# Performance work log

Hardware: AMD Instinct MI355X
Metric: run time of the kernel (lower is better)

## Reference

```python
import jax, jax.numpy as jnp
import numpy as np

B, P = 4, 50000
D_IN, COND = 3, 48
# layer l: in IN_DIMS[l] -> out OUT_DIMS[l]; dims=[3,256*8,257], skip at layer index 4
IN_DIMS  = [D_IN + COND, 256, 256, 256, 256, 256, 256, 256, 256]
OUT_DIMS = [256, 256, 256, 253, 256, 256, 256, 256, 257]
N_LIN = 9
INV_SQRT2 = np.float32(1.0 / np.sqrt(2.0))


def softplus_beta100(x):
    return jax.nn.softplus(100.0 * x) * 0.01


def setup_inputs() -> dict:
    key = jax.random.key(0)
    ks = jax.random.split(key, 2 + 2 * N_LIN)
    inp = {
        "input": jax.random.normal(ks[0], (B, P, D_IN), dtype=jnp.float32),
        "cond_pose": jax.random.normal(ks[1], (B, COND), dtype=jnp.float32),
    }
    for l in range(N_LIN):
        scale = np.float32(np.sqrt(2.0 / OUT_DIMS[l]))  # geometry-style init scale
        inp[f"W{l}"] = jax.random.normal(ks[2 + 2 * l], (OUT_DIMS[l], IN_DIMS[l]), dtype=jnp.float32) * scale
        inp[f"b{l}"] = jnp.zeros((OUT_DIMS[l],), dtype=jnp.float32)
    return inp


def reference(input, cond_pose,
              W0, b0, W1, b1, W2, b2, W3, b3, W4, b4, W5, b5, W6, b6, W7, b7, W8, b8):
    Ws = [W0, W1, W2, W3, W4, W5, W6, W7, W8]
    bs = [b0, b1, b2, b3, b4, b5, b6, b7, b8]
    nb, npnt, nd = input.shape
    x_in = input.reshape(nb * npnt, nd)                                   # (N, 3)
    c = jnp.broadcast_to(cond_pose[:, None, :], (nb, npnt, COND)).reshape(nb * npnt, COND)
    x = jnp.concatenate([x_in, c], axis=-1)                               # cond concat at layer 0
    for l in range(N_LIN):
        if l == 4:  # skip connection: concat raw input, scaled by 1/sqrt(2)
            x = jnp.concatenate([x, x_in], axis=-1) * INV_SQRT2
        x = x @ Ws[l].T + bs[l]
        if l < N_LIN - 1:
            x = softplus_beta100(x)
    return x.reshape(nb, npnt, -1)                                        # (B, P, 257)
```

## Files before the change

kernel.cpp:

```cpp
#include <hip/hip_runtime.h>


typedef __attribute__((ext_vector_type(8))) short bf16x8;
typedef __attribute__((ext_vector_type(4))) float f32x4;
typedef __attribute__((ext_vector_type(2))) float f32x2;

#define PPTS 50000

__device__ __forceinline__ short f2bf(float f) {
    union { float f; unsigned u; } v; v.f = f;
    unsigned r = v.u + 0x7fffu + ((v.u >> 16) & 1u);
    return (short)(r >> 16);
}

__device__ __forceinline__ unsigned cvt_pk_bf16(float lo, float hi) {
    unsigned r;
    asm("v_cvt_pk_bf16_f32 %0, %1, %2" : "=v"(r) : "v"(lo), "v"(hi));
    return r;
}

__device__ __forceinline__ void bar_lgkm() {
    asm volatile("s_waitcnt lgkmcnt(0)" ::: "memory");
    __builtin_amdgcn_s_barrier();
    __builtin_amdgcn_sched_barrier(0);
}

__device__ __forceinline__ f32x2 sp100_pair(f32x2 y) {
    const f32x2 A2 = {6.9314718e-3f, 6.9314718e-3f};
    const f32x2 B2 = {-3.11522e-3f, -3.11522e-3f};
    const f32x2 C2 = {9.8829e-4f,  9.8829e-4f};
    const f32x2 K2 = {-144.26950408889634f, -144.26950408889634f};
    const f32x2 Z2 = {0.0f, 0.0f};
    f32x2 m = __builtin_elementwise_abs(y) * K2;
    f32x2 e = {__builtin_amdgcn_exp2f(m.x), __builtin_amdgcn_exp2f(m.y)};
    f32x2 t = __builtin_elementwise_fma(C2, e, B2);
    t = __builtin_elementwise_fma(t, e, A2);
    return __builtin_elementwise_fma(e, t, __builtin_elementwise_max(y, Z2));
}

__device__ __forceinline__ int xswz(int row) {
    return (((row & 7) ^ (5 * ((row >> 3) & 1))) << 4);
}
__device__ __forceinline__ short* xaddr(short* base, int row, int col) {
    int off = ((row << 9) + (col << 1)) ^ xswz(row);
    return (short*)((char*)base + off);
}
__device__ __forceinline__ const short* xaddrc(const short* base, int row, int col) {
    int off = ((row << 9) + (col << 1)) ^ xswz(row);
    return (const short*)((const char*)base + off);
}

__global__ void prep_kernel(
    const float* __restrict__ W0, const float* __restrict__ W1, const float* __restrict__ W2,
    const float* __restrict__ W3, const float* __restrict__ W4, const float* __restrict__ W5,
    const float* __restrict__ W6, const float* __restrict__ W7, const float* __restrict__ W8,
    short* __restrict__ wbf)
{
    const int gid = blockIdx.x * blockDim.x + threadIdx.x;
    if (gid >= 68096) return;
    int l, cid; const float* Wsrc;
    if      (gid <  2048) { l = 0; cid = gid;         Wsrc = W0; }
    else if (gid < 10240) { l = 1; cid = gid -  2048; Wsrc = W1; }
    else if (gid < 18432) { l = 2; cid = gid - 10240; Wsrc = W2; }
    else if (gid < 26624) { l = 3; cid = gid - 18432; Wsrc = W3; }
    else if (gid < 34816) { l = 4; cid = gid - 26624; Wsrc = W4; }
    else if (gid < 43008) { l = 5; cid = gid - 34816; Wsrc = W5; }
    else if (gid < 51200) { l = 6; cid = gid - 43008; Wsrc = W6; }
    else if (gid < 59392) { l = 7; cid = gid - 51200; Wsrc = W7; }
    else                  { l = 8; cid = gid - 59392; Wsrc = W8; }
    const int NR   = (l == 3) ? 253 : ((l == 8) ? 257 : 256);
    const int KR   = (l == 0) ? 51 : 256;
    const int klog = (l == 0) ? 1 : 3;
    const float sc = (l == 4) ? 0.70710678f : 1.0f;
    const int lane  = cid & 63;
    const int tile  = cid >> 6;
    const int ntile = tile >> klog;
    const int ktile = tile & ((1 << klog) - 1);
    const int n  = ntile * 16 + (lane & 15);
    const int k0 = ktile * 32 + ((lane >> 4) << 3);
    bf16x8 v;
#pragma unroll
    for (int j = 0; j < 8; ++j) {
        int k = k0 + j;
        float f = (n < NR && k < KR) ? Wsrc[n * KR + k] * sc : 0.0f;
        v[j] = f2bf(f);
    }
    ((bf16x8*)wbf)[gid] = v;
}

template<int KSTEPS, int MODE>
__device__ __forceinline__ void layer_fwd(short* xb,
    const bf16x8* __restrict__ wl, const bf16x8* __restrict__ wlnext,
    const float* __restrict__ bias, int lane, int wid, bf16x8 (&apre)[4])
{
    const int prow = lane & 15;
    const int kg   = (lane >> 4) << 3;
    const int rb4  = (lane >> 4) << 2;
    f32x4 acc[4][4];
#pragma unroll
    for (int nii = 0; nii < 4; ++nii) {
        const int cb = (wid * 4 + nii) * 16 + rb4;
        f32x4 bv;
        if (MODE == 1 && cb == 252) { f32x4 tb = {bias[252], 0.f, 0.f, 0.f}; bv = tb; }
        else bv = *(const f32x4*)(bias + cb);
#pragma unroll
        for (int mi = 0; mi < 4; ++mi)
            acc[mi][nii] = bv;
    }
#pragma unroll 2
    for (int ks = 0; ks < KSTEPS; ++ks) {
        bf16x8 a[4], b[4];
#pragma unroll
        for (int nii = 0; nii < 4; ++nii)
            a[nii] = (ks == 0) ? apre[nii]
                               : wl[((wid * 4 + nii) * KSTEPS + ks) * 64 + lane];
#pragma unroll
        for (int mi = 0; mi < 4; ++mi)
            b[mi] = *(const bf16x8*)xaddrc(xb, mi * 16 + prow, ks * 32 + kg);
#pragma unroll
        for (int mi = 0; mi < 4; ++mi)
#pragma unroll
            for (int nii = 0; nii < 4; ++nii)
                acc[mi][nii] = __builtin_amdgcn_mfma_f32_16x16x32_bf16(
                    a[nii], b[mi], acc[mi][nii], 0, 0, 0);
    }
#pragma unroll
    for (int nii = 0; nii < 4; ++nii)
        apre[nii] = wlnext[(wid * 4 + nii) * 512 + lane];
#pragma unroll
    for (int nii = 0; nii < 4; ++nii)
#pragma unroll
        for (int mi = 0; mi < 4; ++mi) {
            f32x2 y0 = {acc[mi][nii][0], acc[mi][nii][1]};
            f32x2 y1 = {acc[mi][nii][2], acc[mi][nii][3]};
            f32x2 r0 = sp100_pair(y0);
            f32x2 r1 = sp100_pair(y1);
            acc[mi][nii][0] = r0.x; acc[mi][nii][1] = r0.y;
            acc[mi][nii][2] = r1.x; acc[mi][nii][3] = r1.y;
        }
    bar_lgkm();
#pragma unroll
    for (int nii = 0; nii < 4; ++nii) {
        const int cb = (wid * 4 + nii) * 16 + rb4;
#pragma unroll
        for (int mi = 0; mi < 4; ++mi) {
            unsigned p01 = cvt_pk_bf16(acc[mi][nii][0], acc[mi][nii][1]);
            unsigned p23 = cvt_pk_bf16(acc[mi][nii][2], acc[mi][nii][3]);
            if (MODE == 1 && cb == 252) {
                *xaddr(xb, mi * 16 + prow, 252) = (short)(p01 & 0xffff);
            } else {
                uint2 pk; pk.x = p01; pk.y = p23;
                *(uint2*)xaddr(xb, mi * 16 + prow, cb) = pk;
            }
        }
    }
}

__global__ __launch_bounds__(256, 3) void net_kernel(
    const float* __restrict__ xin, const float* __restrict__ cond,
    const bf16x8* __restrict__ W,
    const float* __restrict__ b0, const float* __restrict__ b1, const float* __restrict__ b2,
    const float* __restrict__ b3, const float* __restrict__ b4, const float* __restrict__ b5,
    const float* __restrict__ b6, const float* __restrict__ b7, const float* __restrict__ b8,
    float* __restrict__ out)
{
    __shared__ short xb[64 * 256];
    const int t    = threadIdx.x;
    const int pt0  = blockIdx.x * 64;
    const int lane = t & 63;
    const int wid  = t >> 6;

    bf16x8 apre[4];
#pragma unroll
    for (int nii = 0; nii < 4; ++nii)
        apre[nii] = W[(wid * 4 + nii) * 128 + lane];

    float sk[3] = {0.f, 0.f, 0.f};
    if (t < 64) {
#pragma unroll
        for (int c = 0; c < 3; ++c)
            sk[c] = xin[(pt0 + t) * 3 + c];
    }

    {
        const int row   = t >> 2;
        const int c0    = (t & 3) << 4;
        const int point = pt0 + row;
        const int batch = point / PPTS;
        const float* xp = xin + point * 3;
        const float* cp = cond + batch * 48;
#pragma unroll
        for (int h = 0; h < 2; ++h) {
            bf16x8 v;
#pragma unroll
            for (int i = 0; i < 8; ++i) {
                int c = c0 + h * 8 + i;
                float f = (c < 3) ? xp[c] : ((c < 51) ? cp[c - 3] : 0.0f);
                v[i] = f2bf(f);
            }
            *(bf16x8*)xaddr(xb, row, c0 + h * 8) = v;
        }
    }
    bar_lgkm();

    layer_fwd<2, 0>(xb, W +     0, W +  2048, b0, lane, wid, apre); bar_lgkm();
    layer_fwd<8, 0>(xb, W +  2048, W + 10240, b1, lane, wid, apre); bar_lgkm();
    layer_fwd<8, 0>(xb, W + 10240, W + 18432, b2, lane, wid, apre); bar_lgkm();
    layer_fwd<8, 1>(xb, W + 18432, W + 26624, b3, lane, wid, apre);
    if (t < 64) {
#pragma unroll
        for (int c = 0; c < 3; ++c)
            *xaddr(xb, t, 253 + c) = f2bf(sk[c]);
    }
    bar_lgkm();
    layer_fwd<8, 0>(xb, W + 26624, W + 34816, b4, lane, wid, apre); bar_lgkm();
    layer_fwd<8, 0>(xb, W + 34816, W + 43008, b5, lane, wid, apre); bar_lgkm();
    layer_fwd<8, 0>(xb, W + 43008, W + 51200, b6, lane, wid, apre); bar_lgkm();
    layer_fwd<8, 0>(xb, W + 51200, W + 59392, b7, lane, wid, apre); bar_lgkm();

    {
        const bf16x8* wl = W + 59392;
        const int prow = lane & 15;
        const int kg   = (lane >> 4) << 3;
        const int rb4  = (lane >> 4) << 2;
        const float blast = b8[256];
#pragma unroll
        for (int half = 0; half < 2; ++half) {
            f32x4 acc[2][4];
            f32x4 acc2[2];
#pragma unroll
            for (int nii = 0; nii < 4; ++nii) {
                const int cb = (wid * 4 + nii) * 16 + rb4;
                const f32x4 bv = *(const f32x4*)(b8 + cb);
#pragma unroll
                for (int m2 = 0; m2 < 2; ++m2)
                    acc[m2][nii] = bv;
            }
            {
                f32x4 bz = {(rb4 == 0) ? blast : 0.f, 0.f, 0.f, 0.f};
                acc2[0] = bz; acc2[1] = bz;
            }
#pragma unroll 2
            for (int ks = 0; ks < 8; ++ks) {
                bf16x8 a[4], b[2], a2;
#pragma unroll
                for (int nii = 0; nii < 4; ++nii)
                    a[nii] = (half == 0 && ks == 0) ? apre[nii]
                             : wl[((wid * 4 + nii) * 8 + ks) * 64 + lane];
                if (wid == 0) a2 = wl[(128 + ks) * 64 + lane];
#pragma unroll
                for (int m2 = 0; m2 < 2; ++m2)
                    b[m2] = *(const bf16x8*)xaddrc(xb, (half * 2 + m2) * 16 + prow,
                                                   ks * 32 + kg);
#pragma unroll
                for (int m2 = 0; m2 < 2; ++m2)
#pragma unroll
                    for (int nii = 0; nii < 4; ++nii)
                        acc[m2][nii] = __builtin_amdgcn_mfma_f32_16x16x32_bf16(
                            a[nii], b[m2], acc[m2][nii], 0, 0, 0);
                if (wid == 0) {
#pragma unroll
                    for (int m2 = 0; m2 < 2; ++m2)
                        acc2[m2] = __builtin_amdgcn_mfma_f32_16x16x32_bf16(
                            a2, b[m2], acc2[m2], 0, 0, 0);
                }
            }
#pragma unroll
            for (int nii = 0; nii < 4; ++nii) {
                const int cb = (wid * 4 + nii) * 16 + rb4;
#pragma unroll
                for (int m2 = 0; m2 < 2; ++m2) {
                    const int rowoff = (pt0 + (half * 2 + m2) * 16 + prow) * 257 + cb;
#pragma unroll
                    for (int r = 0; r < 4; ++r)
                        out[rowoff + r] = acc[m2][nii][r];
                }
            }
            if (wid == 0 && rb4 == 0) {
#pragma unroll
                for (int m2 = 0; m2 < 2; ++m2)
                    out[(pt0 + (half * 2 + m2) * 16 + prow) * 257 + 256]
                        = acc2[m2][0];
            }
        }
    }
}

extern "C" void kernel_launch(void* const* d_in, const int* in_sizes, int n_in,
                              void* d_out, int out_size, void* d_ws, size_t ws_size,
                              hipStream_t stream)
{
    const float* xin  = (const float*)d_in[0];
    const float* cond = (const float*)d_in[1];
    const float* Wp[9]; const float* bp[9];
    for (int l = 0; l < 9; ++l) { Wp[l] = (const float*)d_in[2 + 2 * l]; bp[l] = (const float*)d_in[3 + 2 * l]; }
    short* wbf = (short*)d_ws;

    prep_kernel<<<dim3(266), dim3(256), 0, stream>>>(
        Wp[0], Wp[1], Wp[2], Wp[3], Wp[4], Wp[5], Wp[6], Wp[7], Wp[8], wbf);
    net_kernel<<<dim3(3125), dim3(256), 0, stream>>>(
        xin, cond, (const bf16x8*)wbf,
        bp[0], bp[1], bp[2], bp[3], bp[4], bp[5], bp[6], bp[7], bp[8],
        (float*)d_out);
}
```

Before: 303.0 us.

## Retile MLP to 128-point blocks with 32x32 MFMA and prefetched weights

Each block now processes 128 points with 512 threads arranged as a 2x4 wave grid. Each wave computes a 64x64 output tile using 32x32x16 bf16 MFMAs instead of 16x16x32, and the weight pre-pack is rearranged to match. Weight fragments for the next k-step are loaded one iteration ahead, and the 257th output column gets its own small 16-wide weight pack handled by one wave column. The aim is more weight reuse per block and fewer MFMA and LDS operations per FLOP. In exchange the block uses 64KB of LDS and more registers, adds bounds clamping for the partial last block, and may reduce occupancy.

```diff
diff --git a/kernel.cpp b/kernel.cpp
--- a/kernel.cpp
+++ b/kernel.cpp
@@ -1,11 +1,13 @@
 #include <hip/hip_runtime.h>
 
 
-typedef __attribute__((ext_vector_type(8))) short bf16x8;
-typedef __attribute__((ext_vector_type(4))) float f32x4;
-typedef __attribute__((ext_vector_type(2))) float f32x2;
+typedef __attribute__((ext_vector_type(8)))  short bf16x8;
+typedef __attribute__((ext_vector_type(16))) float f32x16;
+typedef __attribute__((ext_vector_type(4)))  float f32x4;
+typedef __attribute__((ext_vector_type(2)))  float f32x2;
 
 #define PPTS 50000
+#define NPTS 200000
 
 __device__ __forceinline__ short f2bf(float f) {
     union { float f; unsigned u; } v; v.f = f;
@@ -36,6 +38,14 @@
     f32x2 t = __builtin_elementwise_fma(C2, e, B2);
     t = __builtin_elementwise_fma(t, e, A2);
     return __builtin_elementwise_fma(e, t, __builtin_elementwise_max(y, Z2));
+}
+__device__ __forceinline__ void sp100_16(f32x16& v) {
+#pragma unroll
+    for (int h = 0; h < 8; ++h) {
+        f32x2 y = {v[2*h], v[2*h+1]};
+        f32x2 r = sp100_pair(y);
+        v[2*h] = r.x; v[2*h+1] = r.y;
+    }
 }
 
 __device__ __forceinline__ int xswz(int row) {
@@ -67,96 +77,135 @@
     else if (gid < 43008) { l = 5; cid = gid - 34816; Wsrc = W5; }
     else if (gid < 51200) { l = 6; cid = gid - 43008; Wsrc = W6; }
     else if (gid < 59392) { l = 7; cid = gid - 51200; Wsrc = W7; }
-    else                  { l = 8; cid = gid - 59392; Wsrc = W8; }
-    const int NR   = (l == 3) ? 253 : ((l == 8) ? 257 : 256);
-    const int KR   = (l == 0) ? 51 : 256;
-    const int klog = (l == 0) ? 1 : 3;
-    const float sc = (l == 4) ? 0.70710678f : 1.0f;
-    const int lane  = cid & 63;
-    const int tile  = cid >> 6;
-    const int ntile = tile >> klog;
-    const int ktile = tile & ((1 << klog) - 1);
-    const int n  = ntile * 16 + (lane & 15);
-    const int k0 = ktile * 32 + ((lane >> 4) << 3);
+    else if (gid < 67584) { l = 8; cid = gid - 59392; Wsrc = W8; }
+    else                  { l = 9; cid = gid - 67584; Wsrc = W8; }
+    const int lane = cid & 63;
     bf16x8 v;
-#pragma unroll
-    for (int j = 0; j < 8; ++j) {
-        int k = k0 + j;
-        float f = (n < NR && k < KR) ? Wsrc[n * KR + k] * sc : 0.0f;
-        v[j] = f2bf(f);
+    if (l <= 8) {
+        const int NR   = (l == 3) ? 253 : ((l == 8) ? 257 : 256);
+        const int KR   = (l == 0) ? 51 : 256;
+        const int klog = (l == 0) ? 2 : 4;
+        const float sc = (l == 4) ? 0.70710678f : 1.0f;
+        const int tile = cid >> 6;
+        const int nt   = tile >> klog;
+        const int ks   = tile & ((1 << klog) - 1);
+        const int n  = nt * 32 + (lane & 31);
+        const int k0 = ks * 16 + ((lane >> 5) << 3);
+#pragma unroll
+        for (int j = 0; j < 8; ++j) {
+            int k = k0 + j;
+            float f = (n < NR && k < KR) ? Wsrc[n * KR + k] * sc : 0.0f;
+            v[j] = f2bf(f);
+        }
+    } else {
+        const int ks = cid >> 6;
+        const int n  = 256 + (lane & 15);
+        const int k0 = ks * 32 + ((lane >> 4) << 3);
+#pragma unroll
+        for (int j = 0; j < 8; ++j) {
+            int k = k0 + j;
+            float f = (n < 257) ? Wsrc[n * 256 + k] : 0.0f;
+            v[j] = f2bf(f);
+        }
     }
     ((bf16x8*)wbf)[gid] = v;
 }
 
-template<int KSTEPS, int MODE>
-__device__ __forceinline__ void layer_fwd(short* xb,
+template<int KS, int MODE>
+__device__ __forceinline__ void layer32(short* xb,
     const bf16x8* __restrict__ wl, const bf16x8* __restrict__ wlnext,
-    const float* __restrict__ bias, int lane, int wid, bf16x8 (&apre)[4])
+    const float* __restrict__ bias, int lane, int wr, int wc, bf16x8 (&ap)[2][2])
 {
-    const int prow = lane & 15;
-    const int kg   = (lane >> 4) << 3;
-    const int rb4  = (lane >> 4) << 2;
-    f32x4 acc[4][4];
-#pragma unroll
-    for (int nii = 0; nii < 4; ++nii) {
-        const int cb = (wid * 4 + nii) * 16 + rb4;
-        f32x4 bv;
-        if (MODE == 1 && cb == 252) { f32x4 tb = {bias[252], 0.f, 0.f, 0.f}; bv = tb; }
-        else bv = *(const f32x4*)(bias + cb);
-#pragma unroll
-        for (int mi = 0; mi < 4; ++mi)
-            acc[mi][nii] = bv;
-    }
-#pragma unroll 2
-    for (int ks = 0; ks < KSTEPS; ++ks) {
-        bf16x8 a[4], b[4];
-#pragma unroll
-        for (int nii = 0; nii < 4; ++nii)
-            a[nii] = (ks == 0) ? apre[nii]
-                               : wl[((wid * 4 + nii) * KSTEPS + ks) * 64 + lane];
-#pragma unroll
-        for (int mi = 0; mi < 4; ++mi)
-            b[mi] = *(const bf16x8*)xaddrc(xb, mi * 16 + prow, ks * 32 + kg);
-#pragma unroll
-        for (int mi = 0; mi < 4; ++mi)
-#pragma unroll
-            for (int nii = 0; nii < 4; ++nii)
-                acc[mi][nii] = __builtin_amdgcn_mfma_f32_16x16x32_bf16(
-                    a[nii], b[mi], acc[mi][nii], 0, 0, 0);
-    }
-#pragma unroll
-    for (int nii = 0; nii < 4; ++nii)
-        apre[nii] = wlnext[(wid * 4 + nii) * 512 + lane];
-#pragma unroll
-    for (int nii = 0; nii < 4; ++nii)
-#pragma unroll
-        for (int mi = 0; mi < 4; ++mi) {
-            f32x2 y0 = {acc[mi][nii][0], acc[mi][nii][1]};
-            f32x2 y1 = {acc[mi][nii][2], acc[mi][nii][3]};
-            f32x2 r0 = sp100_pair(y0);
-            f32x2 r1 = sp100_pair(y1);
-            acc[mi][nii][0] = r0.x; acc[mi][nii][1] = r0.y;
-            acc[mi][nii][2] = r1.x; acc[mi][nii][3] = r1.y;
-        }
+    const int p31  = lane & 31;
+    const int hi   = lane >> 5;
+    const int rowb = wr * 64;
+    const int kcol = hi << 3;
+    f32x16 acc[2][2];
+#pragma unroll
+    for (int nt = 0; nt < 2; ++nt) {
+        const int ntb = (wc * 2 + nt) * 32;
+        f32x16 bv;
+#pragma unroll
+        for (int q = 0; q < 4; ++q) {
+            const int cb = ntb + 8 * q + 4 * hi;
+            f32x4 b4;
+            if (MODE == 1 && cb == 252) { f32x4 tb = {bias[252], 0.f, 0.f, 0.f}; b4 = tb; }
+            else b4 = *(const f32x4*)(bias + cb);
+#pragma unroll
+            for (int r = 0; r < 4; ++r) bv[4 * q + r] = b4[r];
+        }
+        acc[0][nt] = bv; acc[1][nt] = bv;
+    }
+    bf16x8 ac[2][2];
+#pragma unroll
+    for (int k2 = 0; k2 < 2; ++k2)
+#pragma unroll
+        for (int nt = 0; nt < 2; ++nt) ac[k2][nt] = ap[k2][nt];
+#pragma unroll
+    for (int p = 0; p < KS / 2; ++p) {
+        bf16x8 an[2][2];
+        if (p + 1 < KS / 2) {
+#pragma unroll
+            for (int k2 = 0; k2 < 2; ++k2)
+#pragma unroll
+                for (int nt = 0; nt < 2; ++nt)
+                    an[k2][nt] = wl[(((wc * 2 + nt) * KS) + 2 * (p + 1) + k2) * 64 + lane];
+        }
+        bf16x8 b[2][2];
+#pragma unroll
+        for (int k2 = 0; k2 < 2; ++k2)
+#pragma unroll
+            for (int mt = 0; mt < 2; ++mt)
+                b[k2][mt] = *(const bf16x8*)xaddrc(xb, rowb + mt * 32 + p31,
+                                                   (2 * p + k2) * 16 + kcol);
+#pragma unroll
+        for (int k2 = 0; k2 < 2; ++k2)
+#pragma unroll
+            for (int mt = 0; mt < 2; ++mt)
+#pragma unroll
+                for (int nt = 0; nt < 2; ++nt)
+                    acc[mt][nt] = __builtin_amdgcn_mfma_f32_32x32x16_bf16(
+                        ac[k2][nt], b[k2][mt], acc[mt][nt], 0, 0, 0);
+        if (p + 1 < KS / 2) {
+#pragma unroll
+            for (int k2 = 0; k2 < 2; ++k2)
+#pragma unroll
+                for (int nt = 0; nt < 2; ++nt) ac[k2][nt] = an[k2][nt];
+        }
+    }
+#pragma unroll
+    for (int k2 = 0; k2 < 2; ++k2)
+#pragma unroll
+        for (int nt = 0; nt < 2; ++nt)
+            ap[k2][nt] = wlnext[(((wc * 2 + nt) * 16) + k2) * 64 + lane];
+#pragma unroll
+    for (int mt = 0; mt < 2; ++mt)
+#pragma unroll
+        for (int nt = 0; nt < 2; ++nt) sp100_16(acc[mt][nt]);
     bar_lgkm();
 #pragma unroll
-    for (int nii = 0; nii < 4; ++nii) {
-        const int cb = (wid * 4 + nii) * 16 + rb4;
-#pragma unroll
-        for (int mi = 0; mi < 4; ++mi) {
-            unsigned p01 = cvt_pk_bf16(acc[mi][nii][0], acc[mi][nii][1]);
-            unsigned p23 = cvt_pk_bf16(acc[mi][nii][2], acc[mi][nii][3]);
-            if (MODE == 1 && cb == 252) {
-                *xaddr(xb, mi * 16 + prow, 252) = (short)(p01 & 0xffff);
-            } else {
-                uint2 pk; pk.x = p01; pk.y = p23;
-                *(uint2*)xaddr(xb, mi * 16 + prow, cb) = pk;
-            }
-        }
-    }
-}
-
-__global__ __launch_bounds__(256, 3) void net_kernel(
+    for (int mt = 0; mt < 2; ++mt) {
+        const int row = rowb + mt * 32 + p31;
+#pragma unroll
+        for (int nt = 0; nt < 2; ++nt) {
+            const int ntb = (wc * 2 + nt) * 32;
+#pragma unroll
+            for (int q = 0; q < 4; ++q) {
+                const int cb = ntb + 8 * q + 4 * hi;
+                unsigned p01 = cvt_pk_bf16(acc[mt][nt][4 * q],     acc[mt][nt][4 * q + 1]);
+                unsigned p23 = cvt_pk_bf16(acc[mt][nt][4 * q + 2], acc[mt][nt][4 * q + 3]);
+                if (MODE == 1 && cb == 252) {
+                    *xaddr(xb, row, 252) = (short)(p01 & 0xffff);
+                } else {
+                    uint2 pk; pk.x = p01; pk.y = p23;
+                    *(uint2*)xaddr(xb, row, cb) = pk;
+                }
+            }
+        }
+    }
+}
+
+__global__ __launch_bounds__(512, 4) void net_kernel(
     const float* __restrict__ xin, const float* __restrict__ cond,
     const bf16x8* __restrict__ W,
     const float* __restrict__ b0, const float* __restrict__ b1, const float* __restrict__ b2,
@@ -164,28 +213,32 @@
     const float* __restrict__ b6, const float* __restrict__ b7, const float* __restrict__ b8,
     float* __restrict__ out)
 {
-    __shared__ short xb[64 * 256];
+    __shared__ short xb[128 * 256];
     const int t    = threadIdx.x;
-    const int pt0  = blockIdx.x * 64;
+    const int pt0  = blockIdx.x * 128;
     const int lane = t & 63;
     const int wid  = t >> 6;
-
-    bf16x8 apre[4];
-#pragma unroll
-    for (int nii = 0; nii < 4; ++nii)
-        apre[nii] = W[(wid * 4 + nii) * 128 + lane];
+    const int wr   = wid >> 2;
+    const int wc   = wid & 3;
+
+    bf16x8 ap[2][2];
+#pragma unroll
+    for (int k2 = 0; k2 < 2; ++k2)
+#pragma unroll
+        for (int nt = 0; nt < 2; ++nt)
+            ap[k2][nt] = W[(((wc * 2 + nt) * 4) + k2) * 64 + lane];
 
     float sk[3] = {0.f, 0.f, 0.f};
-    if (t < 64) {
-#pragma unroll
-        for (int c = 0; c < 3; ++c)
-            sk[c] = xin[(pt0 + t) * 3 + c];
+    if (t < 128) {
+        const int p = min(pt0 + t, NPTS - 1);
+#pragma unroll
+        for (int c = 0; c < 3; ++c) sk[c] = xin[p * 3 + c];
     }
 
     {
         const int row   = t >> 2;
         const int c0    = (t & 3) << 4;
-        const int point = pt0 + row;
+        const int point = min(pt0 + row, NPTS - 1);
         const int batch = point / PPTS;
         const float* xp = xin + point * 3;
         const float* cp = cond + batch * 48;
@@ -203,84 +256,118 @@
     }
     bar_lgkm();
 
-    layer_fwd<2, 0>(xb, W +     0, W +  2048, b0, lane, wid, apre); bar_lgkm();
-    layer_fwd<8, 0>(xb, W +  2048, W + 10240, b1, lane, wid, apre); bar_lgkm();
-    layer_fwd<8, 0>(xb, W + 10240, W + 18432, b2, lane, wid, apre); bar_lgkm();
-    layer_fwd<8, 1>(xb, W + 18432, W + 26624, b3, lane, wid, apre);
-    if (t < 64) {
+    layer32< 4, 0>(xb, W +     0, W +  2048, b0, lane, wr, wc, ap); bar_lgkm();
+    layer32<16, 0>(xb, W +  2048, W + 10240, b1, lane, wr, wc, ap); bar_lgkm();
+    layer32<16, 0>(xb, W + 10240, W + 18432, b2, lane, wr, wc, ap); bar_lgkm();
+    layer32<16, 1>(xb, W + 18432, W + 26624, b3, lane, wr, wc, ap);
+    if (t < 128) {
 #pragma unroll
         for (int c = 0; c < 3; ++c)
             *xaddr(xb, t, 253 + c) = f2bf(sk[c]);
     }
     bar_lgkm();
-    layer_fwd<8, 0>(xb, W + 26624, W + 34816, b4, lane, wid, apre); bar_lgkm();
-    layer_fwd<8, 0>(xb, W + 34816, W + 43008, b5, lane, wid, apre); bar_lgkm();
-    layer_fwd<8, 0>(xb, W + 43008, W + 51200, b6, lane, wid, apre); bar_lgkm();
-    layer_fwd<8, 0>(xb, W + 51200, W + 59392, b7, lane, wid, apre); bar_lgkm();
+    layer32<16, 0>(xb, W + 26624, W + 34816, b4, lane, wr, wc, ap); bar_lgkm();
+    layer32<16, 0>(xb, W + 34816, W + 43008, b5, lane, wr, wc, ap); bar_lgkm();
+    layer32<16, 0>(xb, W + 43008, W + 51200, b6, lane, wr, wc, ap); bar_lgkm();
+    layer32<16, 0>(xb, W + 51200, W + 59392, b7, lane, wr, wc, ap); bar_lgkm();
 
     {
         const bf16x8* wl = W + 59392;
+        const int p31  = lane & 31;
+        const int hi   = lane >> 5;
+        const int rowb = wr * 64;
+        const int kcol = hi << 3;
+        f32x16 acc[2][2];
+#pragma unroll
+        for (int nt = 0; nt < 2; ++nt) {
+            const int ntb = (wc * 2 + nt) * 32;
+            f32x16 bv;
+#pragma unroll
+            for (int q = 0; q < 4; ++q) {
+                const f32x4 b4 = *(const f32x4*)(b8 + ntb + 8 * q + 4 * hi);
+#pragma unroll
+                for (int r = 0; r < 4; ++r) bv[4 * q + r] = b4[r];
+            }
+            acc[0][nt] = bv; acc[1][nt] = bv;
+        }
+        bf16x8 ac[2][2];
+#pragma unroll
+        for (int k2 = 0; k2 < 2; ++k2)
+#pragma unroll
+            for (int nt = 0; nt < 2; ++nt) ac[k2][nt] = ap[k2][nt];
+#pragma unroll
+        for (int p = 0; p < 8; ++p) {
+            bf16x8 an[2][2];
+            if (p < 7) {
+#pragma unroll
+                for (int k2 = 0; k2 < 2; ++k2)
+#pragma unroll
+                    for (int nt = 0; nt < 2; ++nt)
+                        an[k2][nt] = wl[(((wc * 2 + nt) * 16) + 2 * (p + 1) + k2) * 64 + lane];
+            }
+            bf16x8 b[2][2];
+#pragma unroll
+            for (int k2 = 0; k2 < 2; ++k2)
+#pragma unroll
+                for (int mt = 0; mt < 2; ++mt)
+                    b[k2][mt] = *(const bf16x8*)xaddrc(xb, rowb + mt * 32 + p31,
+                                                       (2 * p + k2) * 16 + kcol);
+#pragma unroll
+            for (int k2 = 0; k2 < 2; ++k2)
+#pragma unroll
+                for (int mt = 0; mt < 2; ++mt)
+#pragma unroll
+                    for (int nt = 0; nt < 2; ++nt)
+                        acc[mt][nt] = __builtin_amdgcn_mfma_f32_32x32x16_bf16(
+                            ac[k2][nt], b[k2][mt], acc[mt][nt], 0, 0, 0);
+            if (p < 7) {
+#pragma unroll
+                for (int k2 = 0; k2 < 2; ++k2)
+#pragma unroll
+                    for (int nt = 0; nt < 2; ++nt) ac[k2][nt] = an[k2][nt];
+            }
+        }
+#pragma unroll
+        for (int mt = 0; mt < 2; ++mt) {
+            const int pt = pt0 + rowb + mt * 32 + p31;
+            if (pt < NPTS) {
+#pragma unroll
+                for (int nt = 0; nt < 2; ++nt) {
+                    const int ntb = (wc * 2 + nt) * 32;
+#pragma unroll
+                    for (int q = 0; q < 4; ++q) {
+                        const int cb = ntb + 8 * q + 4 * hi;
+#pragma unroll
+                        for (int r = 0; r < 4; ++r)
+                            out[pt * 257 + cb + r] = acc[mt][nt][4 * q + r];
+                    }
+                }
+            }
+        }
+    }
+    if (wc == 0) {
+        const bf16x8* wt = W + 67584;
         const int prow = lane & 15;
-        const int kg   = (lane >> 4) << 3;
-        const int rb4  = (lane >> 4) << 2;
+        const int rowb = wr * 64;
         const float blast = b8[256];
-#pragma unroll
-        for (int half = 0; half < 2; ++half) {
-            f32x4 acc[2][4];
-            f32x4 acc2[2];
-#pragma unroll
-            for (int nii = 0; nii < 4; ++nii) {
-                const int cb = (wid * 4 + nii) * 16 + rb4;
-                const f32x4 bv = *(const f32x4*)(b8 + cb);
-#pragma unroll
-                for (int m2 = 0; m2 < 2; ++m2)
-                    acc[m2][nii] = bv;
-            }
-            {
-                f32x4 bz = {(rb4 == 0) ? blast : 0.f, 0.f, 0.f, 0.f};
-                acc2[0] = bz; acc2[1] = bz;
-            }
-#pragma unroll 2
-            for (int ks = 0; ks < 8; ++ks) {
-                bf16x8 a[4], b[2], a2;
-#pragma unroll
-                for (int nii = 0; nii < 4; ++nii)
-                    a[nii] = (half == 0 && ks == 0) ? apre[nii]
-                             : wl[((wid * 4 + nii) * 8 + ks) * 64 + lane];
-                if (wid == 0) a2 = wl[(128 + ks) * 64 + lane];
-#pragma unroll
-                for (int m2 = 0; m2 < 2; ++m2)
-                    b[m2] = *(const bf16x8*)xaddrc(xb, (half * 2 + m2) * 16 + prow,
-                                                   ks * 32 + kg);
-#pragma unroll
-                for (int m2 = 0; m2 < 2; ++m2)
-#pragma unroll
-                    for (int nii = 0; nii < 4; ++nii)
-                        acc[m2][nii] = __builtin_amdgcn_mfma_f32_16x16x32_bf16(
-                            a[nii], b[m2], acc[m2][nii], 0, 0, 0);
-                if (wid == 0) {
-#pragma unroll
-                    for (int m2 = 0; m2 < 2; ++m2)
-                        acc2[m2] = __builtin_amdgcn_mfma_f32_16x16x32_bf16(
-                            a2, b[m2], acc2[m2], 0, 0, 0);
-                }
-            }
-#pragma unroll
-            for (int nii = 0; nii < 4; ++nii) {
-                const int cb = (wid * 4 + nii) * 16 + rb4;
-#pragma unroll
-                for (int m2 = 0; m2 < 2; ++m2) {
-                    const int rowoff = (pt0 + (half * 2 + m2) * 16 + prow) * 257 + cb;
-#pragma unroll
-                    for (int r = 0; r < 4; ++r)
-                        out[rowoff + r] = acc[m2][nii][r];
-                }
-            }
-            if (wid == 0 && rb4 == 0) {
-#pragma unroll
-                for (int m2 = 0; m2 < 2; ++m2)
-                    out[(pt0 + (half * 2 + m2) * 16 + prow) * 257 + 256]
-                        = acc2[m2][0];
+        f32x4 acc2[4];
+#pragma unroll
+        for (int mi = 0; mi < 4; ++mi) { f32x4 z = {blast, 0.f, 0.f, 0.f}; acc2[mi] = z; }
+#pragma unroll
+        for (int ks = 0; ks < 8; ++ks) {
+            const bf16x8 a2 = wt[ks * 64 + lane];
+#pragma unroll
+            for (int mi = 0; mi < 4; ++mi) {
+                const bf16x8 bb = *(const bf16x8*)xaddrc(xb, rowb + mi * 16 + prow,
+                                                         ks * 32 + ((lane >> 4) << 3));
+                acc2[mi] = __builtin_amdgcn_mfma_f32_16x16x32_bf16(a2, bb, acc2[mi], 0, 0, 0);
+            }
+        }
+        if ((lane >> 4) == 0) {
+#pragma unroll
+            for (int mi = 0; mi < 4; ++mi) {
+                const int pt = pt0 + rowb + mi * 16 + prow;
+                if (pt < NPTS) out[pt * 257 + 256] = acc2[mi][0];
             }
         }
     }
@@ -298,7 +385,7 @@
 
     prep_kernel<<<dim3(266), dim3(256), 0, stream>>>(
         Wp[0], Wp[1], Wp[2], Wp[3], Wp[4], Wp[5], Wp[6], Wp[7], Wp[8], wbf);
-    net_kernel<<<dim3(3125), dim3(256), 0, stream>>>(
+    net_kernel<<<dim3(1563), dim3(512), 0, stream>>>(
         xin, cond, (const bf16x8*)wbf,
         bp[0], bp[1], bp[2], bp[3], bp[4], bp[5], bp[6], bp[7], bp[8],
         (float*)d_out);
```

Result: slower. 578.1 us (+90.8%).

## Process 128 points per block so each weight fragment feeds twice as many MFMAs

Applied to the files above, without the earlier changes.

Doubles the rows per workgroup from 64 to 128, so each weight fragment loaded from global memory is reused across two 64-row halves with separate accumulators. Next-step weights are software-prefetched one k-step ahead, and the MFMA bursts run at raised wave priority. The final layer's extra output column moves to a separate pass on two waves, and out-of-range points are clamped. The cost is twice the accumulator registers and LDS per block, which lowers occupancy to two blocks per CU, plus a tail block that does partly wasted work.

```diff
diff --git a/kernel.cpp b/kernel.cpp
--- a/kernel.cpp
+++ b/kernel.cpp
@@ -6,6 +6,7 @@
 typedef __attribute__((ext_vector_type(2))) float f32x2;
 
 #define PPTS 50000
+#define NPTS 200000
 
 __device__ __forceinline__ short f2bf(float f) {
     union { float f; unsigned u; } v; v.f = f;
@@ -36,6 +37,11 @@
     f32x2 t = __builtin_elementwise_fma(C2, e, B2);
     t = __builtin_elementwise_fma(t, e, A2);
     return __builtin_elementwise_fma(e, t, __builtin_elementwise_max(y, Z2));
+}
+__device__ __forceinline__ void sp100_4(f32x4& v) {
+    f32x2 y0 = {v[0], v[1]}, y1 = {v[2], v[3]};
+    f32x2 r0 = sp100_pair(y0), r1 = sp100_pair(y1);
+    v[0] = r0.x; v[1] = r0.y; v[2] = r1.x; v[3] = r1.y;
 }
 
 __device__ __forceinline__ int xswz(int row) {
@@ -89,14 +95,14 @@
 }
 
 template<int KSTEPS, int MODE>
-__device__ __forceinline__ void layer_fwd(short* xb,
+__device__ __forceinline__ void layer_dual(short* xb,
     const bf16x8* __restrict__ wl, const bf16x8* __restrict__ wlnext,
-    const float* __restrict__ bias, int lane, int wid, bf16x8 (&apre)[4])
+    const float* __restrict__ bias, int lane, int wid, bf16x8 (&ap)[4])
 {
     const int prow = lane & 15;
     const int kg   = (lane >> 4) << 3;
     const int rb4  = (lane >> 4) << 2;
-    f32x4 acc[4][4];
+    f32x4 accA[4][4], accB[4][4];
 #pragma unroll
     for (int nii = 0; nii < 4; ++nii) {
         const int cb = (wid * 4 + nii) * 16 + rb4;
@@ -104,59 +110,72 @@
         if (MODE == 1 && cb == 252) { f32x4 tb = {bias[252], 0.f, 0.f, 0.f}; bv = tb; }
         else bv = *(const f32x4*)(bias + cb);
 #pragma unroll
+        for (int mi = 0; mi < 4; ++mi) { accA[mi][nii] = bv; accB[mi][nii] = bv; }
+    }
+    bf16x8 a_cur[4];
+#pragma unroll
+    for (int nii = 0; nii < 4; ++nii) a_cur[nii] = ap[nii];
+#pragma unroll
+    for (int ks = 0; ks < KSTEPS; ++ks) {
+        bf16x8 a_nxt[4];
+#pragma unroll
+        for (int nii = 0; nii < 4; ++nii)
+            a_nxt[nii] = (ks + 1 < KSTEPS)
+                ? wl[((wid * 4 + nii) * KSTEPS + ks + 1) * 64 + lane]
+                : wlnext[(wid * 4 + nii) * 512 + lane];
+        bf16x8 bA[4], bB[4];
+#pragma unroll
+        for (int mi = 0; mi < 4; ++mi) {
+            bA[mi] = *(const bf16x8*)xaddrc(xb,      mi * 16 + prow, ks * 32 + kg);
+            bB[mi] = *(const bf16x8*)xaddrc(xb, 64 + mi * 16 + prow, ks * 32 + kg);
+        }
+        __builtin_amdgcn_s_setprio(1);
+#pragma unroll
         for (int mi = 0; mi < 4; ++mi)
-            acc[mi][nii] = bv;
-    }
-#pragma unroll 2
-    for (int ks = 0; ks < KSTEPS; ++ks) {
-        bf16x8 a[4], b[4];
-#pragma unroll
-        for (int nii = 0; nii < 4; ++nii)
-            a[nii] = (ks == 0) ? apre[nii]
-                               : wl[((wid * 4 + nii) * KSTEPS + ks) * 64 + lane];
+#pragma unroll
+            for (int nii = 0; nii < 4; ++nii)
+                accA[mi][nii] = __builtin_amdgcn_mfma_f32_16x16x32_bf16(
+                    a_cur[nii], bA[mi], accA[mi][nii], 0, 0, 0);
 #pragma unroll
         for (int mi = 0; mi < 4; ++mi)
-            b[mi] = *(const bf16x8*)xaddrc(xb, mi * 16 + prow, ks * 32 + kg);
-#pragma unroll
-        for (int mi = 0; mi < 4; ++mi)
 #pragma unroll
             for (int nii = 0; nii < 4; ++nii)
-                acc[mi][nii] = __builtin_amdgcn_mfma_f32_16x16x32_bf16(
-                    a[nii], b[mi], acc[mi][nii], 0, 0, 0);
-    }
+                accB[mi][nii] = __builtin_amdgcn_mfma_f32_16x16x32_bf16(
+                    a_cur[nii], bB[mi], accB[mi][nii], 0, 0, 0);
+        __builtin_amdgcn_s_setprio(0);
+#pragma unroll
+        for (int nii = 0; nii < 4; ++nii) a_cur[nii] = a_nxt[nii];
+    }
+#pragma unroll
+    for (int nii = 0; nii < 4; ++nii) ap[nii] = a_cur[nii];
 #pragma unroll
     for (int nii = 0; nii < 4; ++nii)
-        apre[nii] = wlnext[(wid * 4 + nii) * 512 + lane];
-#pragma unroll
-    for (int nii = 0; nii < 4; ++nii)
-#pragma unroll
-        for (int mi = 0; mi < 4; ++mi) {
-            f32x2 y0 = {acc[mi][nii][0], acc[mi][nii][1]};
-            f32x2 y1 = {acc[mi][nii][2], acc[mi][nii][3]};
-            f32x2 r0 = sp100_pair(y0);
-            f32x2 r1 = sp100_pair(y1);
-            acc[mi][nii][0] = r0.x; acc[mi][nii][1] = r0.y;
-            acc[mi][nii][2] = r1.x; acc[mi][nii][3] = r1.y;
-        }
+#pragma unroll
+        for (int mi = 0; mi < 4; ++mi) { sp100_4(accA[mi][nii]); sp100_4(accB[mi][nii]); }
     bar_lgkm();
 #pragma unroll
     for (int nii = 0; nii < 4; ++nii) {
         const int cb = (wid * 4 + nii) * 16 + rb4;
 #pragma unroll
         for (int mi = 0; mi < 4; ++mi) {
-            unsigned p01 = cvt_pk_bf16(acc[mi][nii][0], acc[mi][nii][1]);
-            unsigned p23 = cvt_pk_bf16(acc[mi][nii][2], acc[mi][nii][3]);
+            unsigned a01 = cvt_pk_bf16(accA[mi][nii][0], accA[mi][nii][1]);
+            unsigned a23 = cvt_pk_bf16(accA[mi][nii][2], accA[mi][nii][3]);
+            unsigned b01 = cvt_pk_bf16(accB[mi][nii][0], accB[mi][nii][1]);
+            unsigned b23 = cvt_pk_bf16(accB[mi][nii][2], accB[mi][nii][3]);
             if (MODE == 1 && cb == 252) {
-                *xaddr(xb, mi * 16 + prow, 252) = (short)(p01 & 0xffff);
+                *xaddr(xb,      mi * 16 + prow, 252) = (short)(a01 & 0xffff);
+                *xaddr(xb, 64 + mi * 16 + prow, 252) = (short)(b01 & 0xffff);
             } else {
-                uint2 pk; pk.x = p01; pk.y = p23;
-                *(uint2*)xaddr(xb, mi * 16 + prow, cb) = pk;
-            }
-        }
-    }
-}
-
-__global__ __launch_bounds__(256, 3) void net_kernel(
+                uint2 pA; pA.x = a01; pA.y = a23;
+                uint2 pB; pB.x = b01; pB.y = b23;
+                *(uint2*)xaddr(xb,      mi * 16 + prow, cb) = pA;
+                *(uint2*)xaddr(xb, 64 + mi * 16 + prow, cb) = pB;
+            }
+        }
+    }
+}
+
+__global__ __launch_bounds__(256, 2) void net_kernel(
     const float* __restrict__ xin, const float* __restrict__ cond,
     const bf16x8* __restrict__ W,
     const float* __restrict__ b0, const float* __restrict__ b1, const float* __restrict__ b2,
@@ -164,33 +183,33 @@
     const float* __restrict__ b6, const float* __restrict__ b7, const float* __restrict__ b8,
     float* __restrict__ out)
 {
-    __shared__ short xb[64 * 256];
+    __shared__ short xb[128 * 256];
     const int t    = threadIdx.x;
-    const int pt0  = blockIdx.x * 64;
+    const int pt0  = blockIdx.x * 128;
     const int lane = t & 63;
     const int wid  = t >> 6;
 
-    bf16x8 apre[4];
+    bf16x8 ap[4];
 #pragma unroll
     for (int nii = 0; nii < 4; ++nii)
-        apre[nii] = W[(wid * 4 + nii) * 128 + lane];
+        ap[nii] = W[(wid * 4 + nii) * 128 + lane];
 
     float sk[3] = {0.f, 0.f, 0.f};
-    if (t < 64) {
-#pragma unroll
-        for (int c = 0; c < 3; ++c)
-            sk[c] = xin[(pt0 + t) * 3 + c];
+    if (t < 128) {
+        const int p = min(pt0 + t, NPTS - 1);
+#pragma unroll
+        for (int c = 0; c < 3; ++c) sk[c] = xin[p * 3 + c];
     }
 
     {
-        const int row   = t >> 2;
-        const int c0    = (t & 3) << 4;
-        const int point = pt0 + row;
+        const int row   = t >> 1;
+        const int c0    = (t & 1) << 5;
+        const int point = min(pt0 + row, NPTS - 1);
         const int batch = point / PPTS;
         const float* xp = xin + point * 3;
         const float* cp = cond + batch * 48;
 #pragma unroll
-        for (int h = 0; h < 2; ++h) {
+        for (int h = 0; h < 4; ++h) {
             bf16x8 v;
 #pragma unroll
             for (int i = 0; i < 8; ++i) {
@@ -203,84 +222,114 @@
     }
     bar_lgkm();
 
-    layer_fwd<2, 0>(xb, W +     0, W +  2048, b0, lane, wid, apre); bar_lgkm();
-    layer_fwd<8, 0>(xb, W +  2048, W + 10240, b1, lane, wid, apre); bar_lgkm();
-    layer_fwd<8, 0>(xb, W + 10240, W + 18432, b2, lane, wid, apre); bar_lgkm();
-    layer_fwd<8, 1>(xb, W + 18432, W + 26624, b3, lane, wid, apre);
-    if (t < 64) {
+    layer_dual<2, 0>(xb, W +     0, W +  2048, b0, lane, wid, ap); bar_lgkm();
+    layer_dual<8, 0>(xb, W +  2048, W + 10240, b1, lane, wid, ap); bar_lgkm();
+    layer_dual<8, 0>(xb, W + 10240, W + 18432, b2, lane, wid, ap); bar_lgkm();
+    layer_dual<8, 1>(xb, W + 18432, W + 26624, b3, lane, wid, ap);
+    if (t < 128) {
 #pragma unroll
         for (int c = 0; c < 3; ++c)
             *xaddr(xb, t, 253 + c) = f2bf(sk[c]);
     }
     bar_lgkm();
-    layer_fwd<8, 0>(xb, W + 26624, W + 34816, b4, lane, wid, apre); bar_lgkm();
-    layer_fwd<8, 0>(xb, W + 34816, W + 43008, b5, lane, wid, apre); bar_lgkm();
-    layer_fwd<8, 0>(xb, W + 43008, W + 51200, b6, lane, wid, apre); bar_lgkm();
-    layer_fwd<8, 0>(xb, W + 51200, W + 59392, b7, lane, wid, apre); bar_lgkm();
+    layer_dual<8, 0>(xb, W + 26624, W + 34816, b4, lane, wid, ap); bar_lgkm();
+    layer_dual<8, 0>(xb, W + 34816, W + 43008, b5, lane, wid, ap); bar_lgkm();
+    layer_dual<8, 0>(xb, W + 43008, W + 51200, b6, lane, wid, ap); bar_lgkm();
+    layer_dual<8, 0>(xb, W + 51200, W + 59392, b7, lane, wid, ap); bar_lgkm();
 
     {
         const bf16x8* wl = W + 59392;
         const int prow = lane & 15;
         const int kg   = (lane >> 4) << 3;
         const int rb4  = (lane >> 4) << 2;
+        f32x4 accA[4][4], accB[4][4];
+#pragma unroll
+        for (int nii = 0; nii < 4; ++nii) {
+            const int cb = (wid * 4 + nii) * 16 + rb4;
+            const f32x4 bv = *(const f32x4*)(b8 + cb);
+#pragma unroll
+            for (int mi = 0; mi < 4; ++mi) { accA[mi][nii] = bv; accB[mi][nii] = bv; }
+        }
+        bf16x8 a_cur[4];
+#pragma unroll
+        for (int nii = 0; nii < 4; ++nii) a_cur[nii] = ap[nii];
+#pragma unroll
+        for (int ks = 0; ks < 8; ++ks) {
+            bf16x8 a_nxt[4];
+            if (ks < 7) {
+#pragma unroll
+                for (int nii = 0; nii < 4; ++nii)
+                    a_nxt[nii] = wl[((wid * 4 + nii) * 8 + ks + 1) * 64 + lane];
+            }
+            bf16x8 bA[4], bB[4];
+#pragma unroll
+            for (int mi = 0; mi < 4; ++mi) {
+                bA[mi] = *(const bf16x8*)xaddrc(xb,      mi * 16 + prow, ks * 32 + kg);
+                bB[mi] = *(const bf16x8*)xaddrc(xb, 64 + mi * 16 + prow, ks * 32 + kg);
+            }
+            __builtin_amdgcn_s_setprio(1);
+#pragma unroll
+            for (int mi = 0; mi < 4; ++mi)
+#pragma unroll
+                for (int nii = 0; nii < 4; ++nii)
+                    accA[mi][nii] = __builtin_amdgcn_mfma_f32_16x16x32_bf16(
+                        a_cur[nii], bA[mi], accA[mi][nii], 0, 0, 0);
+#pragma unroll
+            for (int mi = 0; mi < 4; ++mi)
+#pragma unroll
+                for (int nii = 0; nii < 4; ++nii)
+                    accB[mi][nii] = __builtin_amdgcn_mfma_f32_16x16x32_bf16(
+                        a_cur[nii], bB[mi], accB[mi][nii], 0, 0, 0);
+            __builtin_amdgcn_s_setprio(0);
+            if (ks < 7) {
+#pragma unroll
+                for (int nii = 0; nii < 4; ++nii) a_cur[nii] = a_nxt[nii];
+            }
+        }
+#pragma unroll
+        for (int nii = 0; nii < 4; ++nii) {
+            const int cb = (wid * 4 + nii) * 16 + rb4;
+#pragma unroll
+            for (int mi = 0; mi < 4; ++mi) {
+                const int ptA = pt0 + mi * 16 + prow;
+                const int ptB = ptA + 64;
+                if (ptA < NPTS) {
+#pragma unroll
+                    for (int r = 0; r < 4; ++r)
+                        out[ptA * 257 + cb + r] = accA[mi][nii][r];
+                }
+                if (ptB < NPTS) {
+#pragma unroll
+                    for (int r = 0; r < 4; ++r)
+                        out[ptB * 257 + cb + r] = accB[mi][nii][r];
+                }
+            }
+        }
+    }
+    if (wid < 2) {
+        const bf16x8* wl = W + 59392;
+        const int prow = lane & 15;
+        const int kg   = (lane >> 4) << 3;
+        const int rowoff = wid * 64;
         const float blast = b8[256];
-#pragma unroll
-        for (int half = 0; half < 2; ++half) {
-            f32x4 acc[2][4];
-            f32x4 acc2[2];
-#pragma unroll
-            for (int nii = 0; nii < 4; ++nii) {
-                const int cb = (wid * 4 + nii) * 16 + rb4;
-                const f32x4 bv = *(const f32x4*)(b8 + cb);
-#pragma unroll
-                for (int m2 = 0; m2 < 2; ++m2)
-                    acc[m2][nii] = bv;
-            }
-            {
-                f32x4 bz = {(rb4 == 0) ? blast : 0.f, 0.f, 0.f, 0.f};
-                acc2[0] = bz; acc2[1] = bz;
-            }
-#pragma unroll 2
-            for (int ks = 0; ks < 8; ++ks) {
-                bf16x8 a[4], b[2], a2;
-#pragma unroll
-                for (int nii = 0; nii < 4; ++nii)
-                    a[nii] = (half == 0 && ks == 0) ? apre[nii]
-                             : wl[((wid * 4 + nii) * 8 + ks) * 64 + lane];
-                if (wid == 0) a2 = wl[(128 + ks) * 64 + lane];
-#pragma unroll
-                for (int m2 = 0; m2 < 2; ++m2)
-                    b[m2] = *(const bf16x8*)xaddrc(xb, (half * 2 + m2) * 16 + prow,
-                                                   ks * 32 + kg);
-#pragma unroll
-                for (int m2 = 0; m2 < 2; ++m2)
-#pragma unroll
-                    for (int nii = 0; nii < 4; ++nii)
-                        acc[m2][nii] = __builtin_amdgcn_mfma_f32_16x16x32_bf16(
-                            a[nii], b[m2], acc[m2][nii], 0, 0, 0);
-                if (wid == 0) {
-#pragma unroll
-                    for (int m2 = 0; m2 < 2; ++m2)
-                        acc2[m2] = __builtin_amdgcn_mfma_f32_16x16x32_bf16(
-                            a2, b[m2], acc2[m2], 0, 0, 0);
-                }
-            }
-#pragma unroll
-            for (int nii = 0; nii < 4; ++nii) {
-                const int cb = (wid * 4 + nii) * 16 + rb4;
-#pragma unroll
-                for (int m2 = 0; m2 < 2; ++m2) {
-                    const int rowoff = (pt0 + (half * 2 + m2) * 16 + prow) * 257 + cb;
-#pragma unroll
-                    for (int r = 0; r < 4; ++r)
-                        out[rowoff + r] = acc[m2][nii][r];
-                }
-            }
-            if (wid == 0 && rb4 == 0) {
-#pragma unroll
-                for (int m2 = 0; m2 < 2; ++m2)
-                    out[(pt0 + (half * 2 + m2) * 16 + prow) * 257 + 256]
-                        = acc2[m2][0];
+        f32x4 acc2[4];
+#pragma unroll
+        for (int mi = 0; mi < 4; ++mi) { f32x4 z = {blast, 0.f, 0.f, 0.f}; acc2[mi] = z; }
+#pragma unroll
+        for (int ks = 0; ks < 8; ++ks) {
+            const bf16x8 a2 = wl[(128 + ks) * 64 + lane];
+#pragma unroll
+            for (int mi = 0; mi < 4; ++mi) {
+                const bf16x8 bb = *(const bf16x8*)xaddrc(xb, rowoff + mi * 16 + prow,
+                                                         ks * 32 + kg);
+                acc2[mi] = __builtin_amdgcn_mfma_f32_16x16x32_bf16(a2, bb, acc2[mi], 0, 0, 0);
+            }
+        }
+        if ((lane >> 4) == 0) {
+#pragma unroll
+            for (int mi = 0; mi < 4; ++mi) {
+                const int pt = pt0 + rowoff + mi * 16 + prow;
+                if (pt < NPTS) out[pt * 257 + 256] = acc2[mi][0];
             }
         }
     }
@@ -298,7 +347,7 @@
 
     prep_kernel<<<dim3(266), dim3(256), 0, stream>>>(
         Wp[0], Wp[1], Wp[2], Wp[3], Wp[4], Wp[5], Wp[6], Wp[7], Wp[8], wbf);
-    net_kernel<<<dim3(3125), dim3(256), 0, stream>>>(
+    net_kernel<<<dim3(1563), dim3(256), 0, stream>>>(
         xin, cond, (const bf16x8*)wbf,
         bp[0], bp[1], bp[2], bp[3], bp[4], bp[5], bp[6], bp[7], bp[8],
         (float*)d_out);
```

Result: slower. 766.7 us (+153.0%).

## Software-pipeline MFMA operand loads with register double buffering and setprio

Applied to the files above, without the earlier changes.

Restructures the K loop of each layer so the weight and LDS activation operands for step ks+1 are loaded into a second register set while the MFMAs for step ks run. The next layer's first weight fragment is now fetched inside the final iteration instead of after the loop. The loop is fully unrolled, and the MFMA block is wrapped in s_setprio to favour matrix issue. Occupancy in launch_bounds drops from 3 to 2 blocks per SM to make room for the extra registers, which trades latency hiding across waves for overlap inside each wave.

```diff
diff --git a/kernel.cpp b/kernel.cpp
--- a/kernel.cpp
+++ b/kernel.cpp
@@ -36,6 +36,11 @@
     f32x2 t = __builtin_elementwise_fma(C2, e, B2);
     t = __builtin_elementwise_fma(t, e, A2);
     return __builtin_elementwise_fma(e, t, __builtin_elementwise_max(y, Z2));
+}
+__device__ __forceinline__ void sp100_4(f32x4& v) {
+    f32x2 y0 = {v[0], v[1]}, y1 = {v[2], v[3]};
+    f32x2 r0 = sp100_pair(y0), r1 = sp100_pair(y1);
+    v[0] = r0.x; v[1] = r0.y; v[2] = r1.x; v[3] = r1.y;
 }
 
 __device__ __forceinline__ int xswz(int row) {
@@ -91,7 +96,7 @@
 template<int KSTEPS, int MODE>
 __device__ __forceinline__ void layer_fwd(short* xb,
     const bf16x8* __restrict__ wl, const bf16x8* __restrict__ wlnext,
-    const float* __restrict__ bias, int lane, int wid, bf16x8 (&apre)[4])
+    const float* __restrict__ bias, int lane, int wid, bf16x8 (&ap)[4])
 {
     const int prow = lane & 15;
     const int kg   = (lane >> 4) << 3;
@@ -107,37 +112,50 @@
         for (int mi = 0; mi < 4; ++mi)
             acc[mi][nii] = bv;
     }
-#pragma unroll 2
+    bf16x8 a_cur[4], b_cur[4];
+#pragma unroll
+    for (int nii = 0; nii < 4; ++nii) a_cur[nii] = ap[nii];
+#pragma unroll
+    for (int mi = 0; mi < 4; ++mi)
+        b_cur[mi] = *(const bf16x8*)xaddrc(xb, mi * 16 + prow, kg);
+#pragma unroll
     for (int ks = 0; ks < KSTEPS; ++ks) {
-        bf16x8 a[4], b[4];
-#pragma unroll
-        for (int nii = 0; nii < 4; ++nii)
-            a[nii] = (ks == 0) ? apre[nii]
-                               : wl[((wid * 4 + nii) * KSTEPS + ks) * 64 + lane];
-#pragma unroll
-        for (int mi = 0; mi < 4; ++mi)
-            b[mi] = *(const bf16x8*)xaddrc(xb, mi * 16 + prow, ks * 32 + kg);
+        bf16x8 a_nxt[4], b_nxt[4];
+        if (ks + 1 < KSTEPS) {
+#pragma unroll
+            for (int nii = 0; nii < 4; ++nii)
+                a_nxt[nii] = wl[((wid * 4 + nii) * KSTEPS + ks + 1) * 64 + lane];
+#pragma unroll
+            for (int mi = 0; mi < 4; ++mi)
+                b_nxt[mi] = *(const bf16x8*)xaddrc(xb, mi * 16 + prow,
+                                                   (ks + 1) * 32 + kg);
+        } else {
+#pragma unroll
+            for (int nii = 0; nii < 4; ++nii)
+                a_nxt[nii] = wlnext[(wid * 4 + nii) * 512 + lane];
+        }
+        __builtin_amdgcn_s_setprio(1);
 #pragma unroll
         for (int mi = 0; mi < 4; ++mi)
 #pragma unroll
             for (int nii = 0; nii < 4; ++nii)
                 acc[mi][nii] = __builtin_amdgcn_mfma_f32_16x16x32_bf16(
-                    a[nii], b[mi], acc[mi][nii], 0, 0, 0);
-    }
+                    a_cur[nii], b_cur[mi], acc[mi][nii], 0, 0, 0);
+        __builtin_amdgcn_s_setprio(0);
+#pragma unroll
+        for (int nii = 0; nii < 4; ++nii) a_cur[nii] = a_nxt[nii];
+        if (ks + 1 < KSTEPS) {
+#pragma unroll
+            for (int mi = 0; mi < 4; ++mi) b_cur[mi] = b_nxt[mi];
+        }
+    }
+#pragma unroll
+    for (int nii = 0; nii < 4; ++nii) ap[nii] = a_cur[nii];
 #pragma unroll
     for (int nii = 0; nii < 4; ++nii)
-        apre[nii] = wlnext[(wid * 4 + nii) * 512 + lane];
-#pragma unroll
-    for (int nii = 0; nii < 4; ++nii)
-#pragma unroll
-        for (int mi = 0; mi < 4; ++mi) {
-            f32x2 y0 = {acc[mi][nii][0], acc[mi][nii][1]};
-            f32x2 y1 = {acc[mi][nii][2], acc[mi][nii][3]};
-            f32x2 r0 = sp100_pair(y0);
-            f32x2 r1 = sp100_pair(y1);
-            acc[mi][nii][0] = r0.x; acc[mi][nii][1] = r0.y;
-            acc[mi][nii][2] = r1.x; acc[mi][nii][3] = r1.y;
-        }
+#pragma unroll
+        for (int mi = 0; mi < 4; ++mi)
+            sp100_4(acc[mi][nii]);
     bar_lgkm();
 #pragma unroll
     for (int nii = 0; nii < 4; ++nii) {
@@ -156,7 +174,7 @@
     }
 }
 
-__global__ __launch_bounds__(256, 3) void net_kernel(
+__global__ __launch_bounds__(256, 2) void net_kernel(
     const float* __restrict__ xin, const float* __restrict__ cond,
     const bf16x8* __restrict__ W,
     const float* __restrict__ b0, const float* __restrict__ b1, const float* __restrict__ b2,
@@ -170,10 +188,10 @@
     const int lane = t & 63;
     const int wid  = t >> 6;
 
-    bf16x8 apre[4];
+    bf16x8 ap[4];
 #pragma unroll
     for (int nii = 0; nii < 4; ++nii)
-        apre[nii] = W[(wid * 4 + nii) * 128 + lane];
+        ap[nii] = W[(wid * 4 + nii) * 128 + lane];
 
     float sk[3] = {0.f, 0.f, 0.f};
     if (t < 64) {
@@ -203,20 +221,20 @@
     }
     bar_lgkm();
 
-    layer_fwd<2, 0>(xb, W +     0, W +  2048, b0, lane, wid, apre); bar_lgkm();
-    layer_fwd<8, 0>(xb, W +  2048, W + 10240, b1, lane, wid, apre); bar_lgkm();
-    layer_fwd<8, 0>(xb, W + 10240, W + 18432, b2, lane, wid, apre); bar_lgkm();
-    layer_fwd<8, 1>(xb, W + 18432, W + 26624, b3, lane, wid, apre);
+    layer_fwd<2, 0>(xb, W +     0, W +  2048, b0, lane, wid, ap); bar_lgkm();
+    layer_fwd<8, 0>(xb, W +  2048, W + 10240, b1, lane, wid, ap); bar_lgkm();
+    layer_fwd<8, 0>(xb, W + 10240, W + 18432, b2, lane, wid, ap); bar_lgkm();
+    layer_fwd<8, 1>(xb, W + 18432, W + 26624, b3, lane, wid, ap);
     if (t < 64) {
 #pragma unroll
         for (int c = 0; c < 3; ++c)
             *xaddr(xb, t, 253 + c) = f2bf(sk[c]);
     }
     bar_lgkm();
-    layer_fwd<8, 0>(xb, W + 26624, W + 34816, b4, lane, wid, apre); bar_lgkm();
-    layer_fwd<8, 0>(xb, W + 34816, W + 43008, b5, lane, wid, apre); bar_lgkm();
-    layer_fwd<8, 0>(xb, W + 43008, W + 51200, b6, lane, wid, apre); bar_lgkm();
-    layer_fwd<8, 0>(xb, W + 51200, W + 59392, b7, lane, wid, apre); bar_lgkm();
+    layer_fwd<8, 0>(xb, W + 26624, W + 34816, b4, lane, wid, ap); bar_lgkm();
+    layer_fwd<8, 0>(xb, W + 34816, W + 43008, b5, lane, wid, ap); bar_lgkm();
+    layer_fwd<8, 0>(xb, W + 43008, W + 51200, b6, lane, wid, ap); bar_lgkm();
+    layer_fwd<8, 0>(xb, W + 51200, W + 59392, b7, lane, wid, ap); bar_lgkm();
 
     {
         const bf16x8* wl = W + 59392;
@@ -240,29 +258,46 @@
                 f32x4 bz = {(rb4 == 0) ? blast : 0.f, 0.f, 0.f, 0.f};
                 acc2[0] = bz; acc2[1] = bz;
             }
-#pragma unroll 2
+            bf16x8 a_cur[4], b_cur[2];
+#pragma unroll
+            for (int nii = 0; nii < 4; ++nii)
+                a_cur[nii] = (half == 0) ? ap[nii]
+                           : wl[((wid * 4 + nii) * 8) * 64 + lane];
+#pragma unroll
+            for (int m2 = 0; m2 < 2; ++m2)
+                b_cur[m2] = *(const bf16x8*)xaddrc(xb, (half * 2 + m2) * 16 + prow, kg);
+#pragma unroll
             for (int ks = 0; ks < 8; ++ks) {
-                bf16x8 a[4], b[2], a2;
-#pragma unroll
-                for (int nii = 0; nii < 4; ++nii)
-                    a[nii] = (half == 0 && ks == 0) ? apre[nii]
-                             : wl[((wid * 4 + nii) * 8 + ks) * 64 + lane];
+                bf16x8 a_nxt[4], b_nxt[2], a2;
+                if (ks < 7) {
+#pragma unroll
+                    for (int nii = 0; nii < 4; ++nii)
+                        a_nxt[nii] = wl[((wid * 4 + nii) * 8 + ks + 1) * 64 + lane];
+#pragma unroll
+                    for (int m2 = 0; m2 < 2; ++m2)
+                        b_nxt[m2] = *(const bf16x8*)xaddrc(xb, (half * 2 + m2) * 16 + prow,
+                                                           (ks + 1) * 32 + kg);
+                }
                 if (wid == 0) a2 = wl[(128 + ks) * 64 + lane];
-#pragma unroll
-                for (int m2 = 0; m2 < 2; ++m2)
-                    b[m2] = *(const bf16x8*)xaddrc(xb, (half * 2 + m2) * 16 + prow,
-                                                   ks * 32 + kg);
+                __builtin_amdgcn_s_setprio(1);
 #pragma unroll
                 for (int m2 = 0; m2 < 2; ++m2)
 #pragma unroll
                     for (int nii = 0; nii < 4; ++nii)
                         acc[m2][nii] = __builtin_amdgcn_mfma_f32_16x16x32_bf16(
-                            a[nii], b[m2], acc[m2][nii], 0, 0, 0);
+                            a_cur[nii], b_cur[m2], acc[m2][nii], 0, 0, 0);
                 if (wid == 0) {
 #pragma unroll
                     for (int m2 = 0; m2 < 2; ++m2)
                         acc2[m2] = __builtin_amdgcn_mfma_f32_16x16x32_bf16(
-                            a2, b[m2], acc2[m2], 0, 0, 0);
+                            a2, b_cur[m2], acc2[m2], 0, 0, 0);
+                }
+                __builtin_amdgcn_s_setprio(0);
+                if (ks < 7) {
+#pragma unroll
+                    for (int nii = 0; nii < 4; ++nii) a_cur[nii] = a_nxt[nii];
+#pragma unroll
+                    for (int m2 = 0; m2 < 2; ++m2)  b_cur[m2]  = b_nxt[m2];
                 }
             }
 #pragma unroll
```

Result: faster. 282.1 us (-6.9%).
